# Optimization experiments

Measured on AMD Instinct MI355X. Metric: run time of the kernel, lower is better.

The kernel has to match this reference:

```python
import jax, jax.numpy as jnp
import numpy as np

N, G, E = 100000, 32768, 1000000
F, H = 64, 64


def _mlp(x, w1, b1, w2, b2):
    # Linear -> SiLU -> Linear (matches nn.Sequential in the torch module)
    return jax.nn.silu(x @ w1 + b1) @ w2 + b2


def setup_inputs() -> dict:
    key = jax.random.key(0)
    ks = jax.random.split(key, 24)

    def lin(k, fan_in, fan_out):
        s = 1.0 / np.sqrt(fan_in)
        kw, kb = jax.random.split(k)
        w = jax.random.uniform(kw, (fan_in, fan_out), jnp.float32, -s, s)
        b = jax.random.uniform(kb, (fan_out,), jnp.float32, -s, s)
        return w, b

    node_w1, node_b1 = lin(ks[0], F, H)
    node_w2, node_b2 = lin(ks[1], H, H)
    edge_w1, edge_b1 = lin(ks[2], 6, H)
    edge_w2, edge_b2 = lin(ks[3], H, H)
    msg_w1, msg_b1 = lin(ks[4], 2 * H, H)
    msg_w2, msg_b2 = lin(ks[5], H, H)
    upd_w1, upd_b1 = lin(ks[6], H, H)
    upd_w2, upd_b2 = lin(ks[7], H, H)

    return {
        "node_features": jax.random.normal(ks[8], (N, F), jnp.float32),
        "node_pos": jax.random.normal(ks[9], (N, 3), jnp.float32),
        "grid_pos": jax.random.normal(ks[10], (G, 3), jnp.float32),
        "orientations": jax.random.normal(ks[11], (N, 3, 3), jnp.float32),
        "edge_index": jnp.stack([
            jax.random.randint(ks[12], (E,), 0, N),
            jax.random.randint(ks[13], (E,), 0, G),
        ]),
        "node_w1": node_w1, "node_b1": node_b1, "node_w2": node_w2, "node_b2": node_b2,
        "edge_w1": edge_w1, "edge_b1": edge_b1, "edge_w2": edge_w2, "edge_b2": edge_b2,
        "msg_w1": msg_w1, "msg_b1": msg_b1, "msg_w2": msg_w2, "msg_b2": msg_b2,
        "upd_w1": upd_w1, "upd_b1": upd_b1, "upd_w2": upd_w2, "upd_b2": upd_b2,
    }


def reference(node_features, node_pos, grid_pos, orientations, edge_index,
              node_w1, node_b1, node_w2, node_b2,
              edge_w1, edge_b1, edge_w2, edge_b2,
              msg_w1, msg_b1, msg_w2, msg_b2,
              upd_w1, upd_b1, upd_w2, upd_b2):
    source, target = edge_index[0], edge_index[1]
    num_grid = grid_pos.shape[0]

    # node MLP
    h_node = _mlp(node_features, node_w1, node_b1, node_w2, node_b2)  # [N,H]

    # per-edge message with orientation-aware projection
    pos_s = node_pos[source]                 # [E,3]
    rel = grid_pos[target] - pos_s           # [E,3]
    # bmm(rel[:,None,:], R[source]).squeeze(1) == einsum ei,eij->ej
    trel = jnp.einsum("ei,eij->ej", rel, orientations[source])
    edge_attr = jnp.concatenate([pos_s, trel], axis=-1)        # [E,6]
    e_feat = _mlp(edge_attr, edge_w1, edge_b1, edge_w2, edge_b2)
    msg_in = jnp.concatenate([h_node[source], e_feat], axis=-1)  # [E,2H]
    messages = _mlp(msg_in, msg_w1, msg_b1, msg_w2, msg_b2)      # [E,H]

    # scatter-mean into grid buckets (mask out-of-range targets)
    valid = (target >= 0) & (target < num_grid)
    idx = jnp.where(valid, target, 0)
    msg_masked = jnp.where(valid[:, None], messages, 0.0)
    sums = jax.ops.segment_sum(msg_masked, idx, num_segments=num_grid)
    cnts = jax.ops.segment_sum(valid.astype(jnp.float32), idx, num_segments=num_grid)
    grid_feat = sums / jnp.maximum(cnts, 1.0)[:, None]

    return _mlp(grid_feat, upd_w1, upd_b1, upd_w2, upd_b2)  # [G,H]
```

## Files before the change

kernel.cpp:

```cpp
#include <hip/hip_runtime.h>
#include <hip/hip_bf16.h>
#include <cstdint>

typedef __attribute__((ext_vector_type(8))) short short8;
typedef __attribute__((ext_vector_type(4))) float f32x4;
typedef unsigned short u16;

__device__ __forceinline__ float b2f(u16 u) {
  union { unsigned int i; float f; } v; v.i = ((unsigned int)u) << 16; return v.f;
}
__device__ __forceinline__ u16 f2b(float f) {
  __hip_bfloat16 h = __float2bfloat16(f);
  union { __hip_bfloat16 h; u16 u; } v; v.h = h; return v.u;
}
__device__ __forceinline__ float silu_f(float x) {
  return x * __builtin_amdgcn_rcpf(1.0f + __expf(-x));
}

__device__ __forceinline__ float loadF(const void* p, long i, int isf32) {
  if (isf32) return ((const float*)p)[i];
  return b2f(((const u16*)p)[i]);
}

__device__ __forceinline__ int sniffbit(u16 u) {
  unsigned e = (u >> 7) & 0xffu;
  return (e >= 0xC0u || (e < 0x40u && (u & 0x7fffu) != 0)) ? 1 : 0;
}

struct Ptrs { const void* p[20]; int n[20]; };

#define FW_EW1 0
#define FW_UW1 384
#define FW_UW2 4480
#define FW_UB1 8576
#define FW_UB2 8640
#define FW_EB1 8704
#define FW_EB2 8768
#define FW_MB1 8832
#define FW_MB2 8896
#define FW_TOTAL 8960

#define IMG_EW2 0
#define IMG_MW1 4608
#define IMG_MW2 13312
#define IMG_TOTAL 17920

#define PREP_BLOCKS 105
#define HIST_BLOCKS 1024

__global__ __launch_bounds__(256) void hist_detect_k(
    Ptrs a, const int* __restrict__ eidx, int* __restrict__ cnt8,
    int* __restrict__ flags, long E, int G)
{
  const int t = threadIdx.x;
  const int b = blockIdx.x;
  if (b < HIST_BLOCKS) {
    int* cs = cnt8 + (size_t)(b & 7) * G;
    long i = (long)b * 256 + t;
    const long stride = (long)HIST_BLOCKS * 256;
    for (; i < E; i += stride) {
      int tg = eidx[E + i];
      if (tg >= 0 && tg < G) atomicAdd(&cs[tg], 1);
    }
    return;
  }
  int j = b - HIST_BLOCKS;
  const u16* q = (const u16*)a.p[j];
  int n = a.n[j];
  int m = n < 4096 ? n : 4096;
  int cnt = 0;
  for (int i = t; i < m; i += 256) cnt += sniffbit(q[i]);
  __shared__ int tot;
  if (t == 0) tot = 0;
  __syncthreads();
  if (cnt) atomicAdd(&tot, cnt);
  __syncthreads();
  if (t == 0) flags[j] = (tot >= 2) ? 1 : 0;
}

__global__ __launch_bounds__(256) void scan_prep_node_k(
    Ptrs a, const int* __restrict__ flags,
    const int* __restrict__ cnt8, int* __restrict__ cursor8,
    int* __restrict__ bsum,
    u16* __restrict__ img, float* __restrict__ fw,
    u16* __restrict__ hout, int nrows, int G, int NB2)
{
  const int t = threadIdx.x;
  const int b = blockIdx.x;

  if (b < NB2) {
    __shared__ int sd[256];
    const long tot = 8L * G;
    long j0 = (long)b * 1024 + (long)t * 4;
    int v[4];
#pragma unroll
    for (int k = 0; k < 4; ++k) {
      long j = j0 + k;
      v[k] = (j < tot) ? cnt8[(size_t)(j & 7) * G + (j >> 3)] : 0;
    }
    int local = v[0] + v[1] + v[2] + v[3];
    sd[t] = local;
    __syncthreads();
    for (int off = 1; off < 256; off <<= 1) {
      int x2 = (t >= off) ? sd[t - off] : 0;
      __syncthreads();
      sd[t] += x2;
      __syncthreads();
    }
    int p = sd[t] - local;
#pragma unroll
    for (int k = 0; k < 4; ++k) {
      long j = j0 + k;
      if (j < tot) cursor8[(size_t)(j & 7) * G + (j >> 3)] = p;
      p += v[k];
    }
    if (t == 255) bsum[b] = sd[255];
    return;
  }

  if (b < NB2 + PREP_BLOCKS) {
    int i = (b - NB2) * 256 + t;
    if (i < IMG_TOTAL) {
      const void* bp; int fl; long si; bool real;
      if (i < IMG_MW1) { int nn = i / 72, k = i % 72; bp = a.p[10]; fl = flags[10]; real = k < 64; si = (long)k * 64 + nn; }
      else if (i < IMG_MW2) { int t2 = i - IMG_MW1; int nn = t2 / 136, k = t2 % 136; bp = a.p[12]; fl = flags[12]; real = k < 128; si = (long)k * 64 + nn; }
      else { int t2 = i - IMG_MW2; int nn = t2 / 72, k = t2 % 72; bp = a.p[14]; fl = flags[14]; real = k < 64; si = (long)k * 64 + nn; }
      u16 val = 0;
      if (real) val = f2b(loadF(bp, si, fl));
      img[i] = val;
    } else if (i < IMG_TOTAL + FW_TOTAL) {
      int j = i - IMG_TOTAL;
      const void* bp; int fl; long si;
      if (j < 384)        { bp = a.p[8];  fl = flags[8];  si = j; }
      else if (j < 4480)  { bp = a.p[16]; fl = flags[16]; si = j - 384; }
      else if (j < 8576)  { bp = a.p[18]; fl = flags[18]; si = j - 4480; }
      else {
        int bb = j - 8576; int seg = bb >> 6; si = bb & 63;
        switch (seg) {
          case 0: bp = a.p[17]; fl = flags[17]; break;
          case 1: bp = a.p[19]; fl = flags[19]; break;
          case 2: bp = a.p[9];  fl = flags[9];  break;
          case 3: bp = a.p[11]; fl = flags[11]; break;
          case 4: bp = a.p[13]; fl = flags[13]; break;
          default: bp = a.p[15]; fl = flags[15]; break;
        }
      }
      fw[j] = loadF(bp, si, fl);
    }
    return;
  }

  __shared__ float xs[64][68];
  __shared__ float w1s[64][68];
  __shared__ float w2s[64][68];
  __shared__ float b1s[64];
  __shared__ float b2s[64];
  const void* x = a.p[0];
  const int xf = flags[0], f1 = flags[4], fb1 = flags[5], f2 = flags[6], fb2 = flags[7];
  const long rbase = (long)(b - NB2 - PREP_BLOCKS) * 64;
  for (int i = t; i < 4096; i += 256) {
    int k = i >> 6, cc = i & 63;
    w1s[k][cc] = loadF(a.p[4], i, f1);
    w2s[k][cc] = loadF(a.p[6], i, f2);
  }
  if (t < 64) { b1s[t] = loadF(a.p[5], t, fb1); b2s[t] = loadF(a.p[7], t, fb2); }
  {
    int row = t >> 2, ch = t & 3;
    long rg = rbase + row;
    if (rg < nrows) {
      if (xf) {
        const float* xp = (const float*)x + rg * 64 + ch * 16;
#pragma unroll
        for (int m = 0; m < 16; ++m) xs[row][ch * 16 + m] = xp[m];
      } else {
        const u16* xp = (const u16*)x + rg * 64 + ch * 16;
#pragma unroll
        for (int m = 0; m < 16; ++m) xs[row][ch * 16 + m] = b2f(xp[m]);
      }
    } else {
#pragma unroll
      for (int m = 0; m < 16; ++m) xs[row][ch * 16 + m] = 0.f;
    }
  }
  __syncthreads();
  const int r0 = (t >> 4) * 4, c0 = (t & 15) * 4;
  float acc[4][4];
#pragma unroll
  for (int i = 0; i < 4; ++i)
#pragma unroll
    for (int j = 0; j < 4; ++j) acc[i][j] = b1s[c0 + j];
  for (int k = 0; k < 64; ++k) {
    float w0 = w1s[k][c0], w1v = w1s[k][c0 + 1], w2v = w1s[k][c0 + 2], w3v = w1s[k][c0 + 3];
#pragma unroll
    for (int i = 0; i < 4; ++i) {
      float av = xs[r0 + i][k];
      acc[i][0] = fmaf(av, w0, acc[i][0]);
      acc[i][1] = fmaf(av, w1v, acc[i][1]);
      acc[i][2] = fmaf(av, w2v, acc[i][2]);
      acc[i][3] = fmaf(av, w3v, acc[i][3]);
    }
  }
  __syncthreads();
#pragma unroll
  for (int i = 0; i < 4; ++i)
#pragma unroll
    for (int j = 0; j < 4; ++j) xs[r0 + i][c0 + j] = silu_f(acc[i][j]);
  __syncthreads();
  float acc2[4][4];
#pragma unroll
  for (int i = 0; i < 4; ++i)
#pragma unroll
    for (int j = 0; j < 4; ++j) acc2[i][j] = b2s[c0 + j];
  for (int k = 0; k < 64; ++k) {
    float w0 = w2s[k][c0], w1v = w2s[k][c0 + 1], w2v = w2s[k][c0 + 2], w3v = w2s[k][c0 + 3];
#pragma unroll
    for (int i = 0; i < 4; ++i) {
      float av = xs[r0 + i][k];
      acc2[i][0] = fmaf(av, w0, acc2[i][0]);
      acc2[i][1] = fmaf(av, w1v, acc2[i][1]);
      acc2[i][2] = fmaf(av, w2v, acc2[i][2]);
      acc2[i][3] = fmaf(av, w3v, acc2[i][3]);
    }
  }
#pragma unroll
  for (int i = 0; i < 4; ++i) {
    long rg = rbase + r0 + i;
    if (rg < nrows) {
#pragma unroll
      for (int j = 0; j < 4; ++j) hout[rg * 64 + c0 + j] = f2b(acc2[i][j]);
    }
  }
}

__global__ __launch_bounds__(256) void scat_k(const int* __restrict__ eidx,
                                              int* __restrict__ cursor8,
                                              const int* __restrict__ bsum,
                                              unsigned int* __restrict__ pkS,
                                              int* __restrict__ evp,
                                              long E, int G, int NB2) {
  __shared__ int bo[256];
  const int t = threadIdx.x;
  int v = (t < NB2) ? bsum[t] : 0;
  bo[t] = v;
  __syncthreads();
  for (int off = 1; off < 256; off <<= 1) {
    int x2 = (t >= off) ? bo[t - off] : 0;
    __syncthreads();
    bo[t] += x2;
    __syncthreads();
  }
  if (blockIdx.x == 0 && t == 0) *evp = bo[NB2 - 1];
  int excl = bo[t] - v;
  __syncthreads();
  bo[t] = excl;
  __syncthreads();
  const int c = blockIdx.x & 7;
  int* cur = cursor8 + (size_t)c * G;
  long i = (long)blockIdx.x * 256 + t;
  const long stride = (long)gridDim.x * 256;
  for (; i < E; i += stride) {
    int tg = eidx[E + i];
    if (tg >= 0 && tg < G) {
      int s = eidx[i];
      long j = ((long)tg << 3) | c;
      int p = atomicAdd(&cur[tg], 1) + bo[j >> 10];
      __builtin_nontemporal_store((unsigned int)s | ((unsigned int)tg << 17), pkS + p);
    }
  }
}

#define ETILES 4

__global__ __launch_bounds__(256, 4) void edge_kernel(
    const void* node_pos, const void* grid_pos, const void* orient,
    const unsigned int* __restrict__ pkS, const int* __restrict__ evp,
    const u16* __restrict__ h_node, const u16* __restrict__ img,
    const float* __restrict__ fw, const int* __restrict__ flags,
    float* __restrict__ sums, int G)
{
  __shared__ __align__(16) u16 pool[4][3328];
  __shared__ float eaf[64][6];
  __shared__ float w1e[6][64];
  __shared__ float biasE[4][64];
  __shared__ int tgt_s[64];

  const int t = threadIdx.x;
  const int pf = flags[1], gf = flags[2], of = flags[3];
  const int Ev = *evp;

  const int lane = t & 63, w = t >> 6;
  const int q = lane >> 4, c = lane & 15;
  const int m0 = w * 16;
  u16 (* __restrict__ ef1w)[72] = (u16 (*)[72])&pool[w][0];
  u16 (* __restrict__ hAw)[136] = (u16 (*)[136])&pool[w][1152];
  float (* __restrict__ msgfw)[66] = (float (*)[66])&pool[w][1152];
  const u16* wE2 = img + IMG_EW2;
  const u16* wM1 = img + IMG_MW1;
  const u16* wM2 = img + IMG_MW2;
  const f32x4 z = {0.f, 0.f, 0.f, 0.f};

  const long blockBase = (long)blockIdx.x * (ETILES * 64);

  unsigned int pkA = 0, pkB = 0, pkC = 0, pkD = 0;
  if (lane < 16) {
    long e0 = blockBase + m0 + lane;
    if (e0 < Ev)       pkA = pkS[e0];
    if (e0 + 64 < Ev)  pkB = pkS[e0 + 64];
    if (e0 + 128 < Ev) pkC = pkS[e0 + 128];
    if (e0 + 192 < Ev) pkD = pkS[e0 + 192];
  }

  float o0, o1, o2, o3, o4, o5, o6, o7, o8;
  short8 hv0, hv1;

  {
    int gs = (int)(pkA & 0x1FFFFu);
    if (lane < 16) {
      o0 = loadF(orient, (long)gs * 9 + 0, of);
      o1 = loadF(orient, (long)gs * 9 + 1, of);
      o2 = loadF(orient, (long)gs * 9 + 2, of);
      o3 = loadF(orient, (long)gs * 9 + 3, of);
      o4 = loadF(orient, (long)gs * 9 + 4, of);
      o5 = loadF(orient, (long)gs * 9 + 5, of);
      o6 = loadF(orient, (long)gs * 9 + 6, of);
      o7 = loadF(orient, (long)gs * 9 + 7, of);
      o8 = loadF(orient, (long)gs * 9 + 8, of);
    }
    unsigned int pks = (unsigned int)__shfl((int)pkA, lane >> 2);
    int ss = (int)(pks & 0x1FFFFu);
    const u16* hp = h_node + (long)ss * 64 + (lane & 3) * 16;
    hv0 = *(const short8*)hp;
    hv1 = *(const short8*)(hp + 8);
  }

  for (int i = t; i < 384; i += 256) w1e[i / 64][i % 64] = fw[FW_EW1 + i];
  { int seg = t >> 6, cc = t & 63; biasE[seg][cc] = fw[FW_EB1 + seg * 64 + cc]; }
  __syncthreads();

  for (int tile = 0; tile < ETILES; ++tile) {
    long base = blockBase + (long)tile * 64;
    if (base >= Ev) break;

    if (lane < 16) {
      long eg = base + m0 + lane;
      int gs = (int)(pkA & 0x1FFFFu);
      int tg = (eg < Ev) ? (int)(pkA >> 17) : -1;
      tgt_s[m0 + lane] = tg;
      int tgc = (tg >= 0) ? tg : 0;
      float ps0 = loadF(node_pos, (long)gs * 3 + 0, pf);
      float ps1 = loadF(node_pos, (long)gs * 3 + 1, pf);
      float ps2 = loadF(node_pos, (long)gs * 3 + 2, pf);
      float rel0 = loadF(grid_pos, (long)tgc * 3 + 0, gf) - ps0;
      float rel1 = loadF(grid_pos, (long)tgc * 3 + 1, gf) - ps1;
      float rel2 = loadF(grid_pos, (long)tgc * 3 + 2, gf) - ps2;
      float tr0 = rel0 * o0; tr0 = fmaf(rel1, o3, tr0); tr0 = fmaf(rel2, o6, tr0);
      float tr1 = rel0 * o1; tr1 = fmaf(rel1, o4, tr1); tr1 = fmaf(rel2, o7, tr1);
      float tr2 = rel0 * o2; tr2 = fmaf(rel1, o5, tr2); tr2 = fmaf(rel2, o8, tr2);
      eaf[m0 + lane][0] = ps0; eaf[m0 + lane][1] = ps1; eaf[m0 + lane][2] = ps2;
      eaf[m0 + lane][3] = tr0; eaf[m0 + lane][4] = tr1; eaf[m0 + lane][5] = tr2;
    }
    {
      int er = lane >> 2, ch = lane & 3;
      *(short8*)&hAw[er][ch * 16] = hv0;
      *(short8*)&hAw[er][ch * 16 + 8] = hv1;
    }
    __builtin_amdgcn_sched_barrier(0);
    asm volatile("s_waitcnt lgkmcnt(0)" ::: "memory");
    __builtin_amdgcn_s_barrier();
    __builtin_amdgcn_sched_barrier(0);

    {
      int e = lane >> 2, c0 = (lane & 3) * 16;
      int eb = m0 + e;
      float a0 = eaf[eb][0], a1 = eaf[eb][1], a2 = eaf[eb][2];
      float a3 = eaf[eb][3], a4 = eaf[eb][4], a5 = eaf[eb][5];
      __align__(16) u16 tmp[16];
#pragma unroll
      for (int j = 0; j < 16; ++j) {
        int cc = c0 + j;
        float acc = biasE[0][cc];
        acc = fmaf(a0, w1e[0][cc], acc);
        acc = fmaf(a1, w1e[1][cc], acc);
        acc = fmaf(a2, w1e[2][cc], acc);
        acc = fmaf(a3, w1e[3][cc], acc);
        acc = fmaf(a4, w1e[4][cc], acc);
        acc = fmaf(a5, w1e[5][cc], acc);
        tmp[j] = f2b(silu_f(acc));
      }
      *(short8*)&ef1w[e][c0] = *(const short8*)tmp;
      *(short8*)&ef1w[e][c0 + 8] = *(const short8*)(tmp + 8);
    }
    __builtin_amdgcn_wave_barrier();
    {
      short8 a0 = *(const short8*)&ef1w[c][q * 8];
      short8 a1 = *(const short8*)&ef1w[c][32 + q * 8];
#pragma unroll
      for (int nt = 0; nt < 4; ++nt) {
        short8 b0 = *(const short8*)&wE2[(nt * 16 + c) * 72 + q * 8];
        short8 b1v = *(const short8*)&wE2[(nt * 16 + c) * 72 + 32 + q * 8];
        f32x4 acc = __builtin_amdgcn_mfma_f32_16x16x32_bf16(a0, b0, z, 0, 0, 0);
        acc = __builtin_amdgcn_mfma_f32_16x16x32_bf16(a1, b1v, acc, 0, 0, 0);
#pragma unroll
        for (int r = 0; r < 4; ++r) {
          int row = q * 4 + r, col = nt * 16 + c;
          hAw[row][64 + col] = f2b(acc[r] + biasE[1][col]);
        }
      }
    }
    __builtin_amdgcn_wave_barrier();
    {
      short8 a0 = *(const short8*)&hAw[c][q * 8];
      short8 a1 = *(const short8*)&hAw[c][32 + q * 8];
      short8 a2 = *(const short8*)&hAw[c][64 + q * 8];
      short8 a3 = *(const short8*)&hAw[c][96 + q * 8];
#pragma unroll
      for (int nt = 0; nt < 4; ++nt) {
        const u16* wp = &wM1[(nt * 16 + c) * 136];
        f32x4 acc = __builtin_amdgcn_mfma_f32_16x16x32_bf16(a0, *(const short8*)(wp + q * 8), z, 0, 0, 0);
        acc = __builtin_amdgcn_mfma_f32_16x16x32_bf16(a1, *(const short8*)(wp + 32 + q * 8), acc, 0, 0, 0);
        acc = __builtin_amdgcn_mfma_f32_16x16x32_bf16(a2, *(const short8*)(wp + 64 + q * 8), acc, 0, 0, 0);
        acc = __builtin_amdgcn_mfma_f32_16x16x32_bf16(a3, *(const short8*)(wp + 96 + q * 8), acc, 0, 0, 0);
#pragma unroll
        for (int r = 0; r < 4; ++r) {
          int row = q * 4 + r, col = nt * 16 + c;
          ef1w[row][col] = f2b(silu_f(acc[r] + biasE[2][col]));
        }
      }
    }
    __builtin_amdgcn_wave_barrier();
    {
      short8 a0 = *(const short8*)&ef1w[c][q * 8];
      short8 a1 = *(const short8*)&ef1w[c][32 + q * 8];
      __builtin_amdgcn_wave_barrier();
#pragma unroll
      for (int nt = 0; nt < 4; ++nt) {
        short8 b0 = *(const short8*)&wM2[(nt * 16 + c) * 72 + q * 8];
        short8 b1v = *(const short8*)&wM2[(nt * 16 + c) * 72 + 32 + q * 8];
        f32x4 acc = __builtin_amdgcn_mfma_f32_16x16x32_bf16(a0, b0, z, 0, 0, 0);
        acc = __builtin_amdgcn_mfma_f32_16x16x32_bf16(a1, b1v, acc, 0, 0, 0);
#pragma unroll
        for (int r = 0; r < 4; ++r) {
          int row = q * 4 + r, col = nt * 16 + c;
          msgfw[row][col] = acc[r] + biasE[3][col];
        }
      }
    }
    __builtin_amdgcn_wave_barrier();

    __builtin_amdgcn_sched_barrier(0);
    if (tile + 1 < ETILES && base + 64 < Ev) {
      int gs2 = (int)(pkB & 0x1FFFFu);
      if (lane < 16) {
        o0 = loadF(orient, (long)gs2 * 9 + 0, of);
        o1 = loadF(orient, (long)gs2 * 9 + 1, of);
        o2 = loadF(orient, (long)gs2 * 9 + 2, of);
        o3 = loadF(orient, (long)gs2 * 9 + 3, of);
        o4 = loadF(orient, (long)gs2 * 9 + 4, of);
        o5 = loadF(orient, (long)gs2 * 9 + 5, of);
        o6 = loadF(orient, (long)gs2 * 9 + 6, of);
        o7 = loadF(orient, (long)gs2 * 9 + 7, of);
        o8 = loadF(orient, (long)gs2 * 9 + 8, of);
      }
      unsigned int pks2 = (unsigned int)__shfl((int)pkB, lane >> 2);
      int ss2 = (int)(pks2 & 0x1FFFFu);
      const u16* hp2 = h_node + (long)ss2 * 64 + (lane & 3) * 16;
      hv0 = *(const short8*)hp2;
      hv1 = *(const short8*)(hp2 + 8);
    }
    __builtin_amdgcn_sched_barrier(0);

    {
      int col = lane;
      int cur = tgt_s[m0];
      float run = msgfw[0][col];
      bool lopen = (m0 == 0) ? true : (tgt_s[m0 - 1] == cur);
#pragma unroll
      for (int r2 = 1; r2 < 16; ++r2) {
        int tg = tgt_s[m0 + r2];
        float v = msgfw[r2][col];
        if (tg == cur) {
          run += v;
        } else {
          if (cur >= 0) {
            if (lopen) unsafeAtomicAdd(&sums[(long)cur * 64 + col], run);
            else sums[(long)cur * 64 + col] = run;
          }
          cur = tg; run = v; lopen = false;
        }
      }
      bool ropen = (m0 + 16 >= 64) ? true : (tgt_s[m0 + 16] == cur);
      if (cur >= 0) {
        if (lopen || ropen) unsafeAtomicAdd(&sums[(long)cur * 64 + col], run);
        else sums[(long)cur * 64 + col] = run;
      }
    }
    __builtin_amdgcn_sched_barrier(0);
    asm volatile("s_waitcnt lgkmcnt(0)" ::: "memory");
    __builtin_amdgcn_s_barrier();
    __builtin_amdgcn_sched_barrier(0);
    pkA = pkB; pkB = pkC; pkC = pkD;
  }
}

__global__ __launch_bounds__(256) void upd_mlp(
    const float* __restrict__ sums, const int* __restrict__ cnt8,
    const float* __restrict__ fw, float* __restrict__ out, int nrows)
{
  __shared__ float xs[64][68];
  __shared__ float w1s[64][68];
  __shared__ float w2s[64][68];
  __shared__ float b1s[64];
  __shared__ float b2s[64];
  const int t = threadIdx.x;
  const long rbase = (long)blockIdx.x * 64;
  for (int i = t; i < 4096; i += 256) {
    int k = i >> 6, cc = i & 63;
    w1s[k][cc] = fw[FW_UW1 + i];
    w2s[k][cc] = fw[FW_UW2 + i];
  }
  if (t < 64) { b1s[t] = fw[FW_UB1 + t]; b2s[t] = fw[FW_UB2 + t]; }
  {
    int row = t >> 2, ch = t & 3;
    long rg = rbase + row;
    if (rg < nrows) {
      int cn = 0;
#pragma unroll
      for (int cc = 0; cc < 8; ++cc) cn += cnt8[(size_t)cc * nrows + rg];
      float inv = 1.0f / fmaxf((float)cn, 1.0f);
      const float* p = sums + rg * 64 + ch * 16;
#pragma unroll
      for (int m = 0; m < 16; ++m) xs[row][ch * 16 + m] = p[m] * inv;
    } else {
#pragma unroll
      for (int m = 0; m < 16; ++m) xs[row][ch * 16 + m] = 0.f;
    }
  }
  __syncthreads();
  const int r0 = (t >> 4) * 4, c0 = (t & 15) * 4;
  float acc[4][4];
#pragma unroll
  for (int i = 0; i < 4; ++i)
#pragma unroll
    for (int j = 0; j < 4; ++j) acc[i][j] = b1s[c0 + j];
  for (int k = 0; k < 64; ++k) {
    float w0 = w1s[k][c0], w1v = w1s[k][c0 + 1], w2v = w1s[k][c0 + 2], w3v = w1s[k][c0 + 3];
#pragma unroll
    for (int i = 0; i < 4; ++i) {
      float av = xs[r0 + i][k];
      acc[i][0] = fmaf(av, w0, acc[i][0]);
      acc[i][1] = fmaf(av, w1v, acc[i][1]);
      acc[i][2] = fmaf(av, w2v, acc[i][2]);
      acc[i][3] = fmaf(av, w3v, acc[i][3]);
    }
  }
  __syncthreads();
#pragma unroll
  for (int i = 0; i < 4; ++i)
#pragma unroll
    for (int j = 0; j < 4; ++j) xs[r0 + i][c0 + j] = silu_f(acc[i][j]);
  __syncthreads();
  float acc2[4][4];
#pragma unroll
  for (int i = 0; i < 4; ++i)
#pragma unroll
    for (int j = 0; j < 4; ++j) acc2[i][j] = b2s[c0 + j];
  for (int k = 0; k < 64; ++k) {
    float w0 = w2s[k][c0], w1v = w2s[k][c0 + 1], w2v = w2s[k][c0 + 2], w3v = w2s[k][c0 + 3];
#pragma unroll
    for (int i = 0; i < 4; ++i) {
      float av = xs[r0 + i][k];
      acc2[i][0] = fmaf(av, w0, acc2[i][0]);
      acc2[i][1] = fmaf(av, w1v, acc2[i][1]);
      acc2[i][2] = fmaf(av, w2v, acc2[i][2]);
      acc2[i][3] = fmaf(av, w3v, acc2[i][3]);
    }
  }
#pragma unroll
  for (int i = 0; i < 4; ++i) {
    long rg = rbase + r0 + i;
    if (rg < nrows) {
#pragma unroll
      for (int j = 0; j < 4; ++j) out[rg * 64 + c0 + j] = acc2[i][j];
    }
  }
}

extern "C" void kernel_launch(void* const* d_in, const int* in_sizes, int n_in,
                              void* d_out, int out_size, void* d_ws, size_t ws_size,
                              hipStream_t stream) {
  const int N = in_sizes[1] / 3;
  const int G = in_sizes[2] / 3;
  const long E = (long)in_sizes[4] / 2;
  const int NB2 = (int)((8L * G + 1023) / 1024);
  const int nodeBlocks = (N + 63) / 64;

  char* ws = (char*)d_ws;
  float* sums = (float*)ws;
  size_t off = (size_t)G * 256;
  int* cnt8 = (int*)(ws + off);     off += (size_t)G * 32;
  int* cursor8 = (int*)(ws + off);  off += (size_t)G * 32;
  int* bsum = (int*)(ws + off);     off += 1024;
  int* evp = (int*)(ws + off);      off += 256;
  int* flags = (int*)(ws + off);    off += 256;
  unsigned int* pkS = (unsigned int*)(ws + off); off += (size_t)E * 4;
  u16* h_node = (u16*)(ws + off);   off += (size_t)N * 128;
  u16* img = (u16*)(ws + off);      off += (size_t)IMG_TOTAL * 2;
  float* fw = (float*)(ws + off);

  hipMemsetAsync(ws, 0, (size_t)G * 288, stream);

  Ptrs a;
  const int map[20] = {0,1,2,3, 5,6,7,8, 9,10,11,12, 13,14,15,16, 17,18,19,20};
  for (int i = 0; i < 20; ++i) { a.p[i] = d_in[map[i]]; a.n[i] = in_sizes[map[i]]; }

  hist_detect_k<<<HIST_BLOCKS + 20, 256, 0, stream>>>(
      a, (const int*)d_in[4], cnt8, flags, E, G);
  scan_prep_node_k<<<NB2 + PREP_BLOCKS + nodeBlocks, 256, 0, stream>>>(
      a, flags, cnt8, cursor8, bsum, img, fw, h_node, N, G, NB2);
  scat_k<<<1024, 256, 0, stream>>>((const int*)d_in[4], cursor8, bsum, pkS, evp, E, G, NB2);
  edge_kernel<<<(int)((E + ETILES * 64 - 1) / (ETILES * 64)), 256, 0, stream>>>(
      d_in[1], d_in[2], d_in[3], pkS, evp, h_node, img, fw, flags, sums, G);
  upd_mlp<<<(G + 63) / 64, 256, 0, stream>>>(sums, cnt8, fw, (float*)d_out, G);
}
```

Before: 481.2 us.

## Make edge tiles wave-independent by removing block barriers and shared edge staging

Each wave now keeps its edge attributes and target indices in registers and passes them with lane shuffles, replacing the shared eaf/tgt_s arrays. That removes both per-tile block-wide barriers. The node_pos and grid_pos gathers are prefetched one tile ahead along with the orientations. Neighbor targets for the segment-boundary tests are read straight from global memory, so waves no longer depend on each other. The cost is extra global loads and higher register pressure, and the boundary-open logic at block edges changes slightly, since a block edge is now treated as open only when targets match.

```diff
diff --git a/kernel.cpp b/kernel.cpp
--- a/kernel.cpp
+++ b/kernel.cpp
@@ -279,10 +279,8 @@
     float* __restrict__ sums, int G)
 {
   __shared__ __align__(16) u16 pool[4][3328];
-  __shared__ float eaf[64][6];
   __shared__ float w1e[6][64];
   __shared__ float biasE[4][64];
-  __shared__ int tgt_s[64];
 
   const int t = threadIdx.x;
   const int pf = flags[1], gf = flags[2], of = flags[3];
@@ -310,12 +308,22 @@
     if (e0 + 192 < Ev) pkD = pkS[e0 + 192];
   }
 
-  float o0, o1, o2, o3, o4, o5, o6, o7, o8;
+  float o0 = 0.f, o1 = 0.f, o2 = 0.f, o3 = 0.f, o4 = 0.f, o5 = 0.f,
+        o6 = 0.f, o7 = 0.f, o8 = 0.f;
+  float ps0 = 0.f, ps1 = 0.f, ps2 = 0.f, gp0 = 0.f, gp1 = 0.f, gp2 = 0.f;
   short8 hv0, hv1;
+  int ptg, ntg;
 
   {
     int gs = (int)(pkA & 0x1FFFFu);
+    int tgc = (int)(pkA >> 17);
     if (lane < 16) {
+      ps0 = loadF(node_pos, (long)gs * 3 + 0, pf);
+      ps1 = loadF(node_pos, (long)gs * 3 + 1, pf);
+      ps2 = loadF(node_pos, (long)gs * 3 + 2, pf);
+      gp0 = loadF(grid_pos, (long)tgc * 3 + 0, gf);
+      gp1 = loadF(grid_pos, (long)tgc * 3 + 1, gf);
+      gp2 = loadF(grid_pos, (long)tgc * 3 + 2, gf);
       o0 = loadF(orient, (long)gs * 9 + 0, of);
       o1 = loadF(orient, (long)gs * 9 + 1, of);
       o2 = loadF(orient, (long)gs * 9 + 2, of);
@@ -331,6 +339,10 @@
     const u16* hp = h_node + (long)ss * 64 + (lane & 3) * 16;
     hv0 = *(const short8*)hp;
     hv1 = *(const short8*)(hp + 8);
+    long gPrev = blockBase + m0 - 1;
+    long gNext = blockBase + m0 + 16;
+    ptg = (gPrev >= 0 && gPrev < Ev) ? (int)(pkS[gPrev] >> 17) : -2;
+    ntg = (gNext < Ev) ? (int)(pkS[gNext] >> 17) : -2;
   }
 
   for (int i = t; i < 384; i += 256) w1e[i / 64][i % 64] = fw[FW_EW1 + i];
@@ -341,39 +353,21 @@
     long base = blockBase + (long)tile * 64;
     if (base >= Ev) break;
 
-    if (lane < 16) {
+    int mytg = -1;
+    {
       long eg = base + m0 + lane;
-      int gs = (int)(pkA & 0x1FFFFu);
-      int tg = (eg < Ev) ? (int)(pkA >> 17) : -1;
-      tgt_s[m0 + lane] = tg;
-      int tgc = (tg >= 0) ? tg : 0;
-      float ps0 = loadF(node_pos, (long)gs * 3 + 0, pf);
-      float ps1 = loadF(node_pos, (long)gs * 3 + 1, pf);
-      float ps2 = loadF(node_pos, (long)gs * 3 + 2, pf);
-      float rel0 = loadF(grid_pos, (long)tgc * 3 + 0, gf) - ps0;
-      float rel1 = loadF(grid_pos, (long)tgc * 3 + 1, gf) - ps1;
-      float rel2 = loadF(grid_pos, (long)tgc * 3 + 2, gf) - ps2;
+      if (lane < 16) mytg = (eg < Ev) ? (int)(pkA >> 17) : -1;
+      float rel0 = gp0 - ps0, rel1 = gp1 - ps1, rel2 = gp2 - ps2;
       float tr0 = rel0 * o0; tr0 = fmaf(rel1, o3, tr0); tr0 = fmaf(rel2, o6, tr0);
       float tr1 = rel0 * o1; tr1 = fmaf(rel1, o4, tr1); tr1 = fmaf(rel2, o7, tr1);
       float tr2 = rel0 * o2; tr2 = fmaf(rel1, o5, tr2); tr2 = fmaf(rel2, o8, tr2);
-      eaf[m0 + lane][0] = ps0; eaf[m0 + lane][1] = ps1; eaf[m0 + lane][2] = ps2;
-      eaf[m0 + lane][3] = tr0; eaf[m0 + lane][4] = tr1; eaf[m0 + lane][5] = tr2;
-    }
-    {
+      int sl = lane >> 2;
+      float a0 = __shfl(ps0, sl), a1 = __shfl(ps1, sl), a2 = __shfl(ps2, sl);
+      float a3 = __shfl(tr0, sl), a4 = __shfl(tr1, sl), a5 = __shfl(tr2, sl);
       int er = lane >> 2, ch = lane & 3;
       *(short8*)&hAw[er][ch * 16] = hv0;
       *(short8*)&hAw[er][ch * 16 + 8] = hv1;
-    }
-    __builtin_amdgcn_sched_barrier(0);
-    asm volatile("s_waitcnt lgkmcnt(0)" ::: "memory");
-    __builtin_amdgcn_s_barrier();
-    __builtin_amdgcn_sched_barrier(0);
-
-    {
-      int e = lane >> 2, c0 = (lane & 3) * 16;
-      int eb = m0 + e;
-      float a0 = eaf[eb][0], a1 = eaf[eb][1], a2 = eaf[eb][2];
-      float a3 = eaf[eb][3], a4 = eaf[eb][4], a5 = eaf[eb][5];
+      int c0 = (lane & 3) * 16;
       __align__(16) u16 tmp[16];
 #pragma unroll
       for (int j = 0; j < 16; ++j) {
@@ -387,8 +381,8 @@
         acc = fmaf(a5, w1e[5][cc], acc);
         tmp[j] = f2b(silu_f(acc));
       }
-      *(short8*)&ef1w[e][c0] = *(const short8*)tmp;
-      *(short8*)&ef1w[e][c0 + 8] = *(const short8*)(tmp + 8);
+      *(short8*)&ef1w[er][c0] = *(const short8*)tmp;
+      *(short8*)&ef1w[er][c0 + 8] = *(const short8*)(tmp + 8);
     }
     __builtin_amdgcn_wave_barrier();
     {
@@ -450,7 +444,14 @@
     __builtin_amdgcn_sched_barrier(0);
     if (tile + 1 < ETILES && base + 64 < Ev) {
       int gs2 = (int)(pkB & 0x1FFFFu);
+      int tgc2 = (int)(pkB >> 17);
       if (lane < 16) {
+        ps0 = loadF(node_pos, (long)gs2 * 3 + 0, pf);
+        ps1 = loadF(node_pos, (long)gs2 * 3 + 1, pf);
+        ps2 = loadF(node_pos, (long)gs2 * 3 + 2, pf);
+        gp0 = loadF(grid_pos, (long)tgc2 * 3 + 0, gf);
+        gp1 = loadF(grid_pos, (long)tgc2 * 3 + 1, gf);
+        gp2 = loadF(grid_pos, (long)tgc2 * 3 + 2, gf);
         o0 = loadF(orient, (long)gs2 * 9 + 0, of);
         o1 = loadF(orient, (long)gs2 * 9 + 1, of);
         o2 = loadF(orient, (long)gs2 * 9 + 2, of);
@@ -471,12 +472,12 @@
 
     {
       int col = lane;
-      int cur = tgt_s[m0];
+      int cur = __shfl(mytg, 0);
       float run = msgfw[0][col];
-      bool lopen = (m0 == 0) ? true : (tgt_s[m0 - 1] == cur);
+      bool lopen = (ptg == cur);
 #pragma unroll
       for (int r2 = 1; r2 < 16; ++r2) {
-        int tg = tgt_s[m0 + r2];
+        int tg = __shfl(mytg, r2);
         float v = msgfw[r2][col];
         if (tg == cur) {
           run += v;
@@ -488,16 +489,20 @@
           cur = tg; run = v; lopen = false;
         }
       }
-      bool ropen = (m0 + 16 >= 64) ? true : (tgt_s[m0 + 16] == cur);
+      bool ropen = (ntg == cur);
       if (cur >= 0) {
         if (lopen || ropen) unsafeAtomicAdd(&sums[(long)cur * 64 + col], run);
         else sums[(long)cur * 64 + col] = run;
       }
     }
-    __builtin_amdgcn_sched_barrier(0);
-    asm volatile("s_waitcnt lgkmcnt(0)" ::: "memory");
-    __builtin_amdgcn_s_barrier();
-    __builtin_amdgcn_sched_barrier(0);
+    __builtin_amdgcn_wave_barrier();
+
+    if (tile + 1 < ETILES && base + 64 < Ev) {
+      long gPrev = base + 64 + m0 - 1;
+      long gNext = base + 64 + m0 + 16;
+      ptg = (gPrev < Ev) ? (int)(pkS[gPrev] >> 17) : -2;
+      ntg = (gNext < Ev) ? (int)(pkS[gNext] >> 17) : -2;
+    }
     pkA = pkB; pkB = pkC; pkC = pkD;
   }
 }
```

New measurement: 446.1 us. 7.3% less time.
